# Kernel tuning notes

Hardware: AMD Instinct MI355X
Metric: run time of the kernel (lower is better)

Reference implementation:

```python
import jax, jax.numpy as jnp
import numpy as np

NB, NLOC, NALL = 1, 1024, 1024
NNEI, A_SEL = 64, 16
N_DIM, E_DIM, A_DIM, AXIS = 128, 64, 32, 4
UPD = 0.1  # update_residual, init 'const'


def _mlp_params(key, din, dout):
    kw, kb = jax.random.split(key)
    s = np.float32(1.0 / np.sqrt(din + dout))
    return (jax.random.normal(kw, (din, dout), jnp.float32) * s,
            jax.random.normal(kb, (dout,), jnp.float32) * s)


def setup_inputs() -> dict:
    key = jax.random.key(0)
    ks = jax.random.split(key, 16)
    inp = {}
    inp['node_ebd_ext'] = jax.random.normal(ks[0], (NB, NALL, N_DIM), jnp.float32)
    inp['edge_ebd'] = jax.random.normal(ks[1], (NB, NLOC, NNEI, E_DIM), jnp.float32)
    inp['h2'] = jax.random.normal(ks[2], (NB, NLOC, NNEI, 3), jnp.float32)
    inp['angle_ebd'] = jax.random.normal(ks[3], (NB, NLOC, A_SEL, A_SEL, A_DIM), jnp.float32)
    inp['nlist'] = jax.random.randint(ks[4], (NB, NLOC, NNEI), 0, NALL)
    inp['nlist_mask'] = jnp.ones((NB, NLOC, NNEI), bool)
    inp['sw'] = jax.random.uniform(ks[5], (NB, NLOC, NNEI), jnp.float32)
    inp['a_nlist_mask'] = jnp.ones((NB, NLOC, A_SEL), bool)
    inp['a_sw'] = jax.random.uniform(ks[6], (NB, NLOC, A_SEL), jnp.float32)
    n_sym_dim = AXIS * (N_DIM + E_DIM)          # 768
    edge_info_dim = 2 * N_DIM + E_DIM           # 320
    angle_dim = A_DIM + N_DIM + 2 * E_DIM       # 288 (a_compress_rate == 0)
    inp['w_node_self'], inp['b_node_self'] = _mlp_params(ks[7], N_DIM, N_DIM)
    inp['w_node_sym'], inp['b_node_sym'] = _mlp_params(ks[8], n_sym_dim, N_DIM)
    inp['w_node_edge'], inp['b_node_edge'] = _mlp_params(ks[9], edge_info_dim, N_DIM)
    inp['w_edge_self'], inp['b_edge_self'] = _mlp_params(ks[10], edge_info_dim, E_DIM)
    inp['w_ea1'], inp['b_ea1'] = _mlp_params(ks[11], angle_dim, E_DIM)
    inp['w_ea2'], inp['b_ea2'] = _mlp_params(ks[12], E_DIM, E_DIM)
    inp['w_angle_self'], inp['b_angle_self'] = _mlp_params(ks[13], angle_dim, A_DIM)
    inp['res_n0'] = UPD * jnp.ones((N_DIM,), jnp.float32)
    inp['res_n1'] = UPD * jnp.ones((N_DIM,), jnp.float32)
    inp['res_n2'] = UPD * jnp.ones((N_DIM,), jnp.float32)
    inp['res_e0'] = UPD * jnp.ones((E_DIM,), jnp.float32)
    inp['res_e1'] = UPD * jnp.ones((E_DIM,), jnp.float32)
    inp['res_a0'] = UPD * jnp.ones((A_DIM,), jnp.float32)
    return inp


def reference(node_ebd_ext, edge_ebd, h2, angle_ebd, nlist, nlist_mask, sw,
              a_nlist_mask, a_sw,
              w_node_self, b_node_self, w_node_sym, b_node_sym,
              w_node_edge, b_node_edge, w_edge_self, b_edge_self,
              w_ea1, b_ea1, w_ea2, b_ea2, w_angle_self, b_angle_self,
              res_n0, res_n1, res_n2, res_e0, res_e1, res_a0):
    act = jax.nn.silu
    nb, nloc, nnei, e_dim = edge_ebd.shape
    n_dim = node_ebd_ext.shape[-1]
    node_ebd = node_ebd_ext[:, :nloc]                      # nb x nloc x n_dim
    msw = nlist_mask.astype(edge_ebd.dtype) * sw           # nb x nloc x nnei

    # --- node self update ---
    node_self = act(node_ebd @ w_node_self + b_node_self)

    # --- gather neighbor node embeddings (nb x nloc x nnei x n_dim) ---
    idx = nlist.reshape(nb, nloc * nnei)
    nei_node = jnp.take_along_axis(node_ebd_ext, idx[:, :, None], axis=1)
    nei_node = nei_node.reshape(nb, nloc, nnei, n_dim)

    # --- symmetrization (GRRG invariants) ---
    inv_sqrt_nnei = 1.0 / np.sqrt(np.float32(nnei))
    def sym(ebd):
        g = ebd * msw[..., None]
        h2g2 = jnp.einsum('blnc,blnd->blcd', h2, g) * inv_sqrt_nnei  # nb,nloc,3,d
        grrg = jnp.einsum('blca,blcd->blad', h2g2[..., :AXIS], h2g2) / 3.0
        return grrg.reshape(nb, nloc, AXIS * ebd.shape[-1])
    node_sym = act(jnp.concatenate([sym(edge_ebd), sym(nei_node)], -1)
                   @ w_node_sym + b_node_sym)

    # --- edge info: [node_i, node_j, edge] (nb x nloc x nnei x 320) ---
    node_i = jnp.broadcast_to(node_ebd[:, :, None], (nb, nloc, nnei, n_dim))
    edge_info = jnp.concatenate([node_i, nei_node, edge_ebd], -1)

    # --- node <- edge message ---
    node_edge = (act(edge_info @ w_node_edge + b_node_edge) * sw[..., None]).sum(2) / nnei

    n_updated = node_ebd + res_n0 * node_self + res_n1 * node_sym + res_n2 * node_edge

    # --- edge self update ---
    edge_self = act(edge_info @ w_edge_self + b_edge_self)

    # --- angle info (nb x nloc x a_sel x a_sel x 288) ---
    ea = edge_ebd[:, :, :A_SEL] * a_nlist_mask.astype(edge_ebd.dtype)[..., None]
    node_a = jnp.broadcast_to(node_ebd[:, :, None, None], (nb, nloc, A_SEL, A_SEL, n_dim))
    ea_i = jnp.broadcast_to(ea[:, :, None], (nb, nloc, A_SEL, A_SEL, e_dim))
    ea_j = jnp.broadcast_to(ea[:, :, :, None], (nb, nloc, A_SEL, A_SEL, e_dim))
    angle_info = jnp.concatenate([angle_ebd, node_a, ea_i, ea_j], -1)

    # --- edge <- angle message ---
    eau = act(angle_info @ w_ea1 + b_ea1)
    weighted = a_sw[:, :, :, None, None] * a_sw[:, :, None, :, None] * eau
    reduced = weighted.sum(3) / np.sqrt(np.float32(A_SEL))   # nb,nloc,a_sel,e_dim
    padded = jnp.concatenate(
        [reduced, jnp.zeros((nb, nloc, nnei - A_SEL, e_dim), edge_ebd.dtype)], 2)
    full_mask = jnp.concatenate(
        [a_nlist_mask, jnp.zeros((nb, nloc, nnei - A_SEL), bool)], -1)
    padded = jnp.where(full_mask[..., None], padded, edge_ebd)  # smooth_edge_update=False
    e_angle = act(padded @ w_ea2 + b_ea2)

    e_updated = edge_ebd + res_e0 * edge_self + res_e1 * e_angle

    # --- angle self update ---
    angle_self = act(angle_info @ w_angle_self + b_angle_self)
    a_updated = angle_ebd + res_a0 * angle_self

    return n_updated, e_updated, a_updated
```

## Files before the change

kernel.cpp:

```cpp
#include <hip/hip_runtime.h>
#include <math.h>


typedef __attribute__((ext_vector_type(8))) __bf16 bf16x8;
typedef __attribute__((ext_vector_type(4))) float f32x4;
typedef __attribute__((ext_vector_type(8))) unsigned short us8;

__device__ __forceinline__ float silu(float x) { return x / (1.0f + __expf(-x)); }
__device__ __forceinline__ unsigned short f2bf(float x) {
    union { float f; unsigned int u; } v; v.f = x;
    unsigned int r = v.u + 0x7fffu + ((v.u >> 16) & 1u);
    return (unsigned short)(r >> 16);
}
__device__ __forceinline__ float bf2f(unsigned short h) {
    union { unsigned int u; float f; } v; v.u = ((unsigned int)h) << 16;
    return v.f;
}
__device__ __forceinline__ f32x4 MFMA(bf16x8 a, bf16x8 b, f32x4 c) {
    return __builtin_amdgcn_mfma_f32_16x16x32_bf16(a, b, c, 0, 0, 0);
}

#define OFF_NE  0
#define OFF_ES  24576
#define OFF_E2  36864
#define OFF_A1  40960
#define OFF_AS  43008
#define OFF_EJ1 44032
#define OFF_EI1 48128
#define OFF_EJ2 52224
#define OFF_EI2 54272
#define WS_UNITS 7040

#define P2_NSB  0
#define P2_NEB  16384
#define P2_ESB  32768
#define P2_NSYM 40960
#define P2_UNITS 17408
#define SCR2_BYTES  278528
#define BASES_BYTES 1310720
#define SYMB_BYTES  1572864
#define WS_NEEDED   3274752

__global__ __launch_bounds__(256) void prepAll(
    const float* __restrict__ w_ne, const float* __restrict__ w_es,
    const float* __restrict__ w_e2, const float* __restrict__ w_a1,
    const float* __restrict__ w_as, const float* __restrict__ w_ns,
    const float* __restrict__ w_nsym,
    unsigned short* __restrict__ wsb, unsigned short* __restrict__ scr2)
{
    if (blockIdx.x < 28) {
        int u = blockIdx.x * 256 + threadIdx.x;
        if (u >= WS_UNITS) return;
        const float* w; int N, k0, KS; int uu = u;
        if (uu < 3072)      { w = w_ne; N = 128; k0 = 128; KS = 6; }
        else if (uu < 4608) { uu -= 3072; w = w_es; N = 64;  k0 = 128; KS = 6; }
        else if (uu < 5120) { uu -= 4608; w = w_e2; N = 64;  k0 = 0;   KS = 2; }
        else if (uu < 5376) { uu -= 5120; w = w_a1; N = 64;  k0 = 0;   KS = 1; }
        else if (uu < 5504) { uu -= 5376; w = w_as; N = 32;  k0 = 0;   KS = 1; }
        else if (uu < 6016) { uu -= 5504; w = w_a1; N = 64;  k0 = 160; KS = 2; }
        else if (uu < 6528) { uu -= 6016; w = w_a1; N = 64;  k0 = 224; KS = 2; }
        else if (uu < 6784) { uu -= 6528; w = w_as; N = 32;  k0 = 160; KS = 2; }
        else                { uu -= 6784; w = w_as; N = 32;  k0 = 224; KS = 2; }
        int lane = uu & 63, rest = uu >> 6;
        int ks = rest % KS, nt = rest / KS;
        int k = k0 + ks * 32 + ((lane >> 4) << 3);
        int n = nt * 16 + (lane & 15);
        us8 o;
        #pragma unroll
        for (int t = 0; t < 8; ++t) o[t] = f2bf(w[(size_t)(k + t) * N + n]);
        *(us8*)&wsb[(size_t)u * 8] = o;
    } else {
        int u = (blockIdx.x - 28) * 256 + threadIdx.x;
        if (u >= P2_UNITS) return;
        const float* w; int N, KS; int uu = u;
        if (uu < 2048)      { w = w_ns;   N = 128; KS = 4; }
        else if (uu < 4096) { uu -= 2048; w = w_ne;   N = 128; KS = 4; }
        else if (uu < 5120) { uu -= 4096; w = w_es;   N = 64;  KS = 4; }
        else                { uu -= 5120; w = w_nsym; N = 128; KS = 24; }
        int lane = uu & 63, rest = uu >> 6;
        int ks = rest % KS, nt = rest / KS;
        int k = ks * 32 + ((lane >> 4) << 3);
        int n = nt * 16 + (lane & 15);
        us8 o;
        #pragma unroll
        for (int t = 0; t < 8; ++t) o[t] = f2bf(w[(size_t)(k + t) * N + n]);
        *(us8*)&scr2[(size_t)u * 8] = o;
    }
}

__global__ __launch_bounds__(256) void kernelBases(
    const float* __restrict__ node_ext, const unsigned short* __restrict__ scr2,
    const float* __restrict__ b_ns, const float* __restrict__ b_ne,
    const float* __restrict__ b_es, float* __restrict__ bases)
{
    __shared__ __align__(16) unsigned short s_N[16][136];
    const int b = blockIdx.x, tid = threadIdx.x, L0 = b * 16;
    for (int v = tid; v < 2048; v += 256)
        s_N[v >> 7][v & 127] = f2bf(node_ext[(size_t)(L0 + (v >> 7)) * 128 + (v & 127)]);
    __syncthreads();
    const int wv = tid >> 6, ln = tid & 63, lg = ln >> 4, lr = ln & 15;
    f32x4 acc[5];
    #pragma unroll
    for (int n = 0; n < 5; ++n) acc[n] = (f32x4){0.f,0.f,0.f,0.f};
    #pragma unroll
    for (int ks = 0; ks < 4; ++ks) {
        bf16x8 a = *(const bf16x8*)&s_N[lr][ks*32 + lg*8];
        #pragma unroll
        for (int ntl = 0; ntl < 5; ++ntl) {
            int t = wv * 5 + ntl;
            size_t eoff;
            if      (t < 8)  eoff = P2_NSB + (size_t)((t*4+ks)*64+ln)*8;
            else if (t < 16) eoff = P2_NEB + (size_t)(((t-8)*4+ks)*64+ln)*8;
            else             eoff = P2_ESB + (size_t)(((t-16)*4+ks)*64+ln)*8;
            bf16x8 bb = *(const bf16x8*)&scr2[eoff];
            acc[ntl] = MFMA(a, bb, acc[ntl]);
        }
    }
    #pragma unroll
    for (int ntl = 0; ntl < 5; ++ntl) {
        int t = wv * 5 + ntl;
        int col = t * 16 + lr;
        float bias = (col < 128) ? b_ns[col] : (col < 256) ? b_ne[col-128] : b_es[col-256];
        #pragma unroll
        for (int r = 0; r < 4; ++r)
            bases[(size_t)(L0 + lg*4 + r) * 320 + col] = acc[ntl][r] + bias;
    }
}

__global__ __launch_bounds__(512, 8) void kernelA(
    const float* __restrict__ node_ext, const float* __restrict__ edge,
    const float* __restrict__ h2, const int* __restrict__ nlist,
    const float* __restrict__ sw, const unsigned short* __restrict__ wsb,
    const float* __restrict__ bases, unsigned short* __restrict__ symb,
    const float* __restrict__ b_ea2,
    const float* __restrict__ res_n0, const float* __restrict__ res_n2,
    const float* __restrict__ res_e0, const float* __restrict__ res_e1,
    float* __restrict__ out_n, float* __restrict__ out_e)
{
    __shared__ __align__(16) unsigned short s_X[64][200];
    __shared__ float s_h2g2[3][192];
    __shared__ float s_base[320];
    __shared__ float s_ne[128];
    __shared__ float s_nodef[128];
    __shared__ float s_sw[64];
    __shared__ float s_h2w[192];
    __shared__ int   s_nl[64];

    const int l = blockIdx.x, tid = threadIdx.x;

    if (tid < 64) {
        s_nl[tid] = nlist[l*64 + tid];
        s_base[256 + tid] = bases[(size_t)l * 320 + 256 + tid];
    }
    else if (tid < 192) s_nodef[tid - 64] = node_ext[(size_t)l*128 + (tid - 64)];
    else if (tid < 256) s_sw[tid - 192] = sw[l*64 + (tid - 192)];
    else s_base[tid - 256] = bases[(size_t)l * 320 + (tid - 256)];
    __syncthreads();

    for (int v = tid; v < 8192; v += 512) {
        int n = v >> 7, j = v & 127;
        s_X[n][j] = f2bf(node_ext[(size_t)s_nl[n] * 128 + j]);
    }
    for (int v = tid; v < 4096; v += 512)
        s_X[v >> 6][128 + (v & 63)] = f2bf(edge[(size_t)l * 4096 + v]);
    if (tid < 192) s_h2w[tid] = h2[(size_t)l * 192 + tid] * s_sw[tid / 3];
    __syncthreads();

    for (int v = tid; v < 576; v += 512) {
        int c = v / 192, d = v % 192;
        float p0 = 0.f, p1 = 0.f, p2 = 0.f, p3 = 0.f;
        for (int n = 0; n < 64; n += 4) {
            p0 = fmaf(s_h2w[n * 3 + c],       bf2f(s_X[n][d]),     p0);
            p1 = fmaf(s_h2w[(n + 1) * 3 + c], bf2f(s_X[n + 1][d]), p1);
            p2 = fmaf(s_h2w[(n + 2) * 3 + c], bf2f(s_X[n + 2][d]), p2);
            p3 = fmaf(s_h2w[(n + 3) * 3 + c], bf2f(s_X[n + 3][d]), p3);
        }
        s_h2g2[c][d] = ((p0 + p1) + (p2 + p3)) * 0.125f;
    }
    __syncthreads();

    const int wv = tid >> 6, ln = tid & 63, lg = ln >> 4, lr = ln & 15;

    {
        f32x4 acc[4];
        #pragma unroll
        for (int m = 0; m < 4; ++m) acc[m] = (f32x4){0.f, 0.f, 0.f, 0.f};
        #pragma unroll
        for (int ks = 0; ks < 6; ++ks) {
            bf16x8 b = *(const bf16x8*)&wsb[OFF_NE + (size_t)((wv * 6 + ks) * 64 + ln) * 8];
            #pragma unroll
            for (int m = 0; m < 4; ++m) {
                bf16x8 a = *(const bf16x8*)&s_X[m * 16 + lr][ks * 32 + lg * 8];
                acc[m] = MFMA(a, b, acc[m]);
            }
        }
        int col = wv * 16 + lr;
        float base = s_base[128 + col];
        float cs = 0.f;
        #pragma unroll
        for (int m = 0; m < 4; ++m)
            #pragma unroll
            for (int r = 0; r < 4; ++r)
                cs = fmaf(silu(base + acc[m][r]), s_sw[m * 16 + lg * 4 + r], cs);
        cs += __shfl_xor(cs, 16);
        cs += __shfl_xor(cs, 32);
        if (lg == 0) s_ne[col] = cs;
    }

    {
        const int nt = wv >> 1, m0 = (wv & 1) * 2;
        f32x4 aes[2], ae2[2];
        #pragma unroll
        for (int mm = 0; mm < 2; ++mm) {
            aes[mm] = (f32x4){0.f, 0.f, 0.f, 0.f};
            ae2[mm] = (f32x4){0.f, 0.f, 0.f, 0.f};
        }
        #pragma unroll
        for (int ks = 0; ks < 6; ++ks) {
            bf16x8 b = *(const bf16x8*)&wsb[OFF_ES + (size_t)((nt * 6 + ks) * 64 + ln) * 8];
            bf16x8 a[2];
            #pragma unroll
            for (int mm = 0; mm < 2; ++mm)
                a[mm] = *(const bf16x8*)&s_X[(m0 + mm) * 16 + lr][ks * 32 + lg * 8];
            #pragma unroll
            for (int mm = 0; mm < 2; ++mm) aes[mm] = MFMA(a[mm], b, aes[mm]);
            if (ks >= 4) {
                bf16x8 b2 = *(const bf16x8*)&wsb[OFF_E2 + (size_t)((nt * 2 + (ks - 4)) * 64 + ln) * 8];
                #pragma unroll
                for (int mm = 0; mm < 2; ++mm)
                    if (m0 + mm > 0) ae2[mm] = MFMA(a[mm], b2, ae2[mm]);
            }
        }
        int o = nt * 16 + lr;
        float esb = s_base[256 + o];
        float re0 = res_e0[o], re1 = res_e1[o], be2 = b_ea2[o];
        #pragma unroll
        for (int mm = 0; mm < 2; ++mm) {
            int m = m0 + mm;
            #pragma unroll
            for (int r = 0; r < 4; ++r) {
                int n = m * 16 + lg * 4 + r;
                size_t gi = (size_t)l * 4096 + (size_t)n * 64 + o;
                float val = bf2f(s_X[n][128 + o]) + re0 * silu(esb + aes[mm][r]);
                if (m > 0) val = fmaf(re1, silu(be2 + ae2[mm][r]), val);
                out_e[gi] = val;
            }
        }
    }

    for (int v = tid; v < 768; v += 512) {
        float p;
        if (v < 256) {
            int a = v >> 6, d = v & 63;
            p = s_h2g2[0][128 + a] * s_h2g2[0][128 + d]
              + s_h2g2[1][128 + a] * s_h2g2[1][128 + d]
              + s_h2g2[2][128 + a] * s_h2g2[2][128 + d];
        } else {
            int v2 = v - 256; int a = v2 >> 7, d = v2 & 127;
            p = s_h2g2[0][a] * s_h2g2[0][d]
              + s_h2g2[1][a] * s_h2g2[1][d]
              + s_h2g2[2][a] * s_h2g2[2][d];
        }
        symb[(size_t)l * 768 + v] = f2bf(p * (1.f / 3.f));
    }
    __syncthreads();

    if (tid < 128) {
        float ne = s_ne[tid] * (1.f / 64.f);
        float v = s_nodef[tid];
        v = fmaf(res_n0[tid], silu(s_base[tid]), v);
        v = fmaf(res_n2[tid], ne, v);
        out_n[(size_t)l * 128 + tid] = v;
    }
}

__global__ __launch_bounds__(256) void kernelNsym(
    const unsigned short* __restrict__ symb, const unsigned short* __restrict__ scr2,
    const float* __restrict__ b_nsym, const float* __restrict__ res_n1,
    float* __restrict__ out_n)
{
    const int b = blockIdx.x, tid = threadIdx.x, L0 = b * 16;
    const int wv = tid >> 6, ln = tid & 63, lg = ln >> 4, lr = ln & 15;
    f32x4 acc[2];
    acc[0] = (f32x4){0.f,0.f,0.f,0.f};
    acc[1] = (f32x4){0.f,0.f,0.f,0.f};
    for (int ks = 0; ks < 24; ++ks) {
        bf16x8 a = *(const bf16x8*)&symb[(size_t)(L0 + lr) * 768 + ks*32 + lg*8];
        #pragma unroll
        for (int nt = 0; nt < 2; ++nt) {
            bf16x8 bb = *(const bf16x8*)&scr2[P2_NSYM + (size_t)(((wv*2+nt)*24+ks)*64+ln)*8];
            acc[nt] = MFMA(a, bb, acc[nt]);
        }
    }
    #pragma unroll
    for (int nt = 0; nt < 2; ++nt) {
        int col = (wv*2 + nt) * 16 + lr;
        float bias = b_nsym[col], rn = res_n1[col];
        #pragma unroll
        for (int r = 0; r < 4; ++r) {
            size_t idx = (size_t)(L0 + lg*4 + r) * 128 + col;
            out_n[idx] += rn * silu(acc[nt][r] + bias);
        }
    }
}

__global__ __launch_bounds__(512, 8) void kernelB(
    const float* __restrict__ node_ext, const float* __restrict__ edge,
    const float* __restrict__ angle, const float* __restrict__ a_sw,
    const unsigned short* __restrict__ wsb,
    const float* __restrict__ w_ea1, const float* __restrict__ b_ea1,
    const float* __restrict__ b_ea2,
    const float* __restrict__ w_angle_self, const float* __restrict__ b_angle_self,
    const float* __restrict__ res_e1, const float* __restrict__ res_a0,
    float* __restrict__ out_e, float* __restrict__ out_a)
{
    __shared__ __align__(16) unsigned short s_ea[16][72];
    __shared__ __align__(16) unsigned short s_redb[16][72];
    __shared__ float s_ej1[16][66];
    __shared__ float s_ei1[16][64];
    __shared__ float s_ej2[16][34];
    __shared__ float s_ei2[16][32];
    __shared__ float s_nt1[64];
    __shared__ float s_nt2[32];
    __shared__ float s_asw[16];
    __shared__ float s_nodef[128];

    const int l = blockIdx.x, tid = threadIdx.x;
    const int wv = tid >> 6, ln = tid & 63, lg = ln >> 4, lr = ln & 15;

    bf16x8 a[2];
    #pragma unroll
    for (int mm = 0; mm < 2; ++mm) {
        const float* ap = angle + (size_t)l * 8192
                        + (size_t)((wv * 2 + mm) * 16 + lr) * 32 + lg * 8;
        float4 f0 = *(const float4*)ap;
        float4 f1 = *(const float4*)(ap + 4);
        bf16x8 t;
        t[0] = (__bf16)f0.x; t[1] = (__bf16)f0.y; t[2] = (__bf16)f0.z; t[3] = (__bf16)f0.w;
        t[4] = (__bf16)f1.x; t[5] = (__bf16)f1.y; t[6] = (__bf16)f1.z; t[7] = (__bf16)f1.w;
        a[mm] = t;
    }

    if (tid < 128) s_nodef[tid] = node_ext[(size_t)l * 128 + tid];
    else if (tid < 144) s_asw[tid - 128] = a_sw[l * 16 + (tid - 128)];
    for (int v = tid; v < 1024; v += 512) s_ea[v >> 6][v & 63] = f2bf(edge[(size_t)l * 4096 + v]);
    __syncthreads();

    if (wv < 6) {
        bf16x8 a0 = *(const bf16x8*)&s_ea[lr][lg * 8];
        bf16x8 a1 = *(const bf16x8*)&s_ea[lr][32 + lg * 8];
        if (wv < 2) {
            #pragma unroll
            for (int ntl = 0; ntl < 2; ++ntl) {
                int nt = wv * 2 + ntl;
                f32x4 c = (f32x4){0.f, 0.f, 0.f, 0.f};
                c = MFMA(a0, *(const bf16x8*)&wsb[OFF_EJ1 + (size_t)((nt * 2 + 0) * 64 + ln) * 8], c);
                c = MFMA(a1, *(const bf16x8*)&wsb[OFF_EJ1 + (size_t)((nt * 2 + 1) * 64 + ln) * 8], c);
                #pragma unroll
                for (int r = 0; r < 4; ++r) s_ej1[lg * 4 + r][nt * 16 + lr] = c[r];
            }
        } else if (wv < 4) {
            #pragma unroll
            for (int ntl = 0; ntl < 2; ++ntl) {
                int nt = (wv - 2) * 2 + ntl;
                f32x4 c = (f32x4){0.f, 0.f, 0.f, 0.f};
                c = MFMA(a0, *(const bf16x8*)&wsb[OFF_EI1 + (size_t)((nt * 2 + 0) * 64 + ln) * 8], c);
                c = MFMA(a1, *(const bf16x8*)&wsb[OFF_EI1 + (size_t)((nt * 2 + 1) * 64 + ln) * 8], c);
                #pragma unroll
                for (int r = 0; r < 4; ++r) s_ei1[lg * 4 + r][nt * 16 + lr] = c[r];
            }
        } else if (wv == 4) {
            #pragma unroll
            for (int nt = 0; nt < 2; ++nt) {
                f32x4 c = (f32x4){0.f, 0.f, 0.f, 0.f};
                c = MFMA(a0, *(const bf16x8*)&wsb[OFF_EJ2 + (size_t)((nt * 2 + 0) * 64 + ln) * 8], c);
                c = MFMA(a1, *(const bf16x8*)&wsb[OFF_EJ2 + (size_t)((nt * 2 + 1) * 64 + ln) * 8], c);
                #pragma unroll
                for (int r = 0; r < 4; ++r) s_ej2[lg * 4 + r][nt * 16 + lr] = c[r];
            }
        } else {
            #pragma unroll
            for (int nt = 0; nt < 2; ++nt) {
                f32x4 c = (f32x4){0.f, 0.f, 0.f, 0.f};
                c = MFMA(a0, *(const bf16x8*)&wsb[OFF_EI2 + (size_t)((nt * 2 + 0) * 64 + ln) * 8], c);
                c = MFMA(a1, *(const bf16x8*)&wsb[OFF_EI2 + (size_t)((nt * 2 + 1) * 64 + ln) * 8], c);
                #pragma unroll
                for (int r = 0; r < 4; ++r) s_ei2[lg * 4 + r][nt * 16 + lr] = c[r];
            }
        }
    } else if (wv == 6) {
        float p = b_ea1[ln];
        for (int k = 0; k < 128; ++k) p = fmaf(s_nodef[k], w_ea1[(32 + k) * 64 + ln], p);
        s_nt1[ln] = p;
    } else {
        if (ln < 32) {
            float p = b_angle_self[ln];
            for (int k = 0; k < 128; ++k) p = fmaf(s_nodef[k], w_angle_self[(32 + k) * 32 + ln], p);
            s_nt2[ln] = p;
        }
    }
    __syncthreads();

    #pragma unroll
    for (int nt = 0; nt < 4; ++nt) {
        bf16x8 b = *(const bf16x8*)&wsb[OFF_A1 + (size_t)(nt * 64 + ln) * 8];
        #pragma unroll
        for (int mm = 0; mm < 2; ++mm) {
            f32x4 c = MFMA(a[mm], b, (f32x4){0.f, 0.f, 0.f, 0.f});
            int i = wv * 2 + mm;
            int o = nt * 16 + lr;
            float b0 = s_nt1[o] + s_ei1[i][o];
            float ps = 0.f;
            #pragma unroll
            for (int r = 0; r < 4; ++r) {
                int jj = lg * 4 + r;
                ps = fmaf(silu(c[r] + b0 + s_ej1[jj][o]), s_asw[jj], ps);
            }
            ps += __shfl_xor(ps, 16);
            ps += __shfl_xor(ps, 32);
            if (lg == 0) s_redb[i][o] = f2bf(ps * s_asw[i] * 0.25f);
        }
    }
    #pragma unroll
    for (int nt = 0; nt < 2; ++nt) {
        bf16x8 b = *(const bf16x8*)&wsb[OFF_AS + (size_t)(nt * 64 + ln) * 8];
        #pragma unroll
        for (int mm = 0; mm < 2; ++mm) {
            f32x4 c = MFMA(a[mm], b, (f32x4){0.f, 0.f, 0.f, 0.f});
            int i = wv * 2 + mm;
            int o = nt * 16 + lr;
            float b0 = s_nt2[o] + s_ei2[i][o];
            float ra = res_a0[o];
            #pragma unroll
            for (int r = 0; r < 4; ++r) {
                int jj = lg * 4 + r;
                size_t gi = (size_t)l * 8192 + (size_t)(i * 16 + jj) * 32 + o;
                out_a[gi] = angle[gi] + ra * silu(c[r] + b0 + s_ej2[jj][o]);
            }
        }
    }
    __syncthreads();

    if (wv < 4) {
        bf16x8 a0 = *(const bf16x8*)&s_redb[lr][lg * 8];
        bf16x8 a1 = *(const bf16x8*)&s_redb[lr][32 + lg * 8];
        const int nt = wv;
        f32x4 c = (f32x4){0.f, 0.f, 0.f, 0.f};
        c = MFMA(a0, *(const bf16x8*)&wsb[OFF_E2 + (size_t)((nt * 2 + 0) * 64 + ln) * 8], c);
        c = MFMA(a1, *(const bf16x8*)&wsb[OFF_E2 + (size_t)((nt * 2 + 1) * 64 + ln) * 8], c);
        int o = nt * 16 + lr;
        float be = b_ea2[o], re1 = res_e1[o];
        #pragma unroll
        for (int r = 0; r < 4; ++r) {
            int n = lg * 4 + r;
            size_t gi = (size_t)l * 4096 + (size_t)n * 64 + o;
            out_e[gi] += re1 * silu(be + c[r]);
        }
    }
}

extern "C" void kernel_launch(void* const* d_in, const int* in_sizes, int n_in,
                              void* d_out, int out_size, void* d_ws, size_t ws_size,
                              hipStream_t stream)
{
    const float* node_ext     = (const float*)d_in[0];
    const float* edge         = (const float*)d_in[1];
    const float* h2           = (const float*)d_in[2];
    const float* angle        = (const float*)d_in[3];
    const int*   nlist        = (const int*)d_in[4];
    const float* sw           = (const float*)d_in[6];
    const float* a_sw         = (const float*)d_in[8];
    const float* w_node_self  = (const float*)d_in[9];
    const float* b_node_self  = (const float*)d_in[10];
    const float* w_node_sym   = (const float*)d_in[11];
    const float* b_node_sym   = (const float*)d_in[12];
    const float* w_node_edge  = (const float*)d_in[13];
    const float* b_node_edge  = (const float*)d_in[14];
    const float* w_edge_self  = (const float*)d_in[15];
    const float* b_edge_self  = (const float*)d_in[16];
    const float* w_ea1        = (const float*)d_in[17];
    const float* b_ea1        = (const float*)d_in[18];
    const float* w_ea2        = (const float*)d_in[19];
    const float* b_ea2        = (const float*)d_in[20];
    const float* w_angle_self = (const float*)d_in[21];
    const float* b_angle_self = (const float*)d_in[22];
    const float* res_n0       = (const float*)d_in[23];
    const float* res_n1       = (const float*)d_in[24];
    const float* res_n2       = (const float*)d_in[25];
    const float* res_e0       = (const float*)d_in[26];
    const float* res_e1       = (const float*)d_in[27];
    const float* res_a0       = (const float*)d_in[28];

    float* out_n = (float*)d_out;
    float* out_e = out_n + 1024 * 128;
    float* out_a = out_e + 1024 * 64 * 64;
    unsigned short* wsb = (unsigned short*)d_ws;

    char* scrbase = (ws_size >= (size_t)WS_NEEDED) ? ((char*)d_ws + 112640)
                                                   : (char*)out_a;
    unsigned short* scr2 = (unsigned short*)scrbase;
    float* bases = (float*)(scrbase + SCR2_BYTES);
    unsigned short* symb = (unsigned short*)(scrbase + SCR2_BYTES + BASES_BYTES);
    (void)in_sizes; (void)n_in; (void)out_size;

    hipLaunchKernelGGL(prepAll, dim3(96), dim3(256), 0, stream,
        w_node_edge, w_edge_self, w_ea2, w_ea1, w_angle_self, w_node_self, w_node_sym,
        wsb, scr2);

    hipLaunchKernelGGL(kernelBases, dim3(64), dim3(256), 0, stream,
        node_ext, scr2, b_node_self, b_node_edge, b_edge_self, bases);

    hipLaunchKernelGGL(kernelA, dim3(1024), dim3(512), 0, stream,
        node_ext, edge, h2, nlist, sw, wsb, bases, symb, b_ea2,
        res_n0, res_n2, res_e0, res_e1, out_n, out_e);

    hipLaunchKernelGGL(kernelNsym, dim3(64), dim3(256), 0, stream,
        symb, scr2, b_node_sym, res_n1, out_n);

    hipLaunchKernelGGL(kernelB, dim3(1024), dim3(512), 0, stream,
        node_ext, edge, angle, a_sw, wsb,
        w_ea1, b_ea1, b_ea2, w_angle_self, b_angle_self,
        res_e1, res_a0, out_e, out_a);
}
```

Baseline: 78.66 us.

## Fold node-sym GEMM into kernelB and precompute per-node angle terms in bases

The per-node angle projection terms (node_ebd @ w_ea1 and node_ebd @ w_angle_self slices) move into the batched MFMA bases kernel, so kernelB no longer runs scalar 128-long dot products in two waves. The separate kernelNsym launch is folded into kernelB as 64 extra blocks, removing one launch, and kernelA gathers with float4 loads. This costs a larger workspace and a fallback path when the workspace is too small, and the extra blocks share kernelB's 512-thread shape and LDS footprint.

After: 81.06 us. 1.03x slower.

```diff
diff --git a/kernel.cpp b/kernel.cpp
--- a/kernel.cpp
+++ b/kernel.cpp
@@ -35,11 +35,13 @@
 #define P2_NEB  16384
 #define P2_ESB  32768
 #define P2_NSYM 40960
-#define P2_UNITS 17408
-#define SCR2_BYTES  278528
-#define BASES_BYTES 1310720
+#define P2_NT1  139264
+#define P2_NT2  147456
+#define P2_UNITS 18944
+#define SCR2_BYTES  303104
+#define BASES_BYTES 1703936
 #define SYMB_BYTES  1572864
-#define WS_NEEDED   3274752
+#define WS_NEEDED   3692544
 
 __global__ __launch_bounds__(256) void prepAll(
     const float* __restrict__ w_ne, const float* __restrict__ w_es,
@@ -72,14 +74,16 @@
     } else {
         int u = (blockIdx.x - 28) * 256 + threadIdx.x;
         if (u >= P2_UNITS) return;
-        const float* w; int N, KS; int uu = u;
-        if (uu < 2048)      { w = w_ns;   N = 128; KS = 4; }
-        else if (uu < 4096) { uu -= 2048; w = w_ne;   N = 128; KS = 4; }
-        else if (uu < 5120) { uu -= 4096; w = w_es;   N = 64;  KS = 4; }
-        else                { uu -= 5120; w = w_nsym; N = 128; KS = 24; }
+        const float* w; int N, k0, KS; int uu = u;
+        if (uu < 2048)       { w = w_ns;   N = 128; k0 = 0;  KS = 4; }
+        else if (uu < 4096)  { uu -= 2048;  w = w_ne;   N = 128; k0 = 0;  KS = 4; }
+        else if (uu < 5120)  { uu -= 4096;  w = w_es;   N = 64;  k0 = 0;  KS = 4; }
+        else if (uu < 17408) { uu -= 5120;  w = w_nsym; N = 128; k0 = 0;  KS = 24; }
+        else if (uu < 18432) { uu -= 17408; w = w_a1;   N = 64;  k0 = 32; KS = 4; }
+        else                 { uu -= 18432; w = w_as;   N = 32;  k0 = 32; KS = 4; }
         int lane = uu & 63, rest = uu >> 6;
         int ks = rest % KS, nt = rest / KS;
-        int k = ks * 32 + ((lane >> 4) << 3);
+        int k = k0 + ks * 32 + ((lane >> 4) << 3);
         int n = nt * 16 + (lane & 15);
         us8 o;
         #pragma unroll
@@ -91,7 +95,8 @@
 __global__ __launch_bounds__(256) void kernelBases(
     const float* __restrict__ node_ext, const unsigned short* __restrict__ scr2,
     const float* __restrict__ b_ns, const float* __restrict__ b_ne,
-    const float* __restrict__ b_es, float* __restrict__ bases)
+    const float* __restrict__ b_es, const float* __restrict__ b_ea1,
+    const float* __restrict__ b_as, float* __restrict__ bases)
 {
     __shared__ __align__(16) unsigned short s_N[16][136];
     const int b = blockIdx.x, tid = threadIdx.x, L0 = b * 16;
@@ -99,31 +104,37 @@
         s_N[v >> 7][v & 127] = f2bf(node_ext[(size_t)(L0 + (v >> 7)) * 128 + (v & 127)]);
     __syncthreads();
     const int wv = tid >> 6, ln = tid & 63, lg = ln >> 4, lr = ln & 15;
-    f32x4 acc[5];
-    #pragma unroll
-    for (int n = 0; n < 5; ++n) acc[n] = (f32x4){0.f,0.f,0.f,0.f};
+    f32x4 acc[7];
+    #pragma unroll
+    for (int n = 0; n < 7; ++n) acc[n] = (f32x4){0.f,0.f,0.f,0.f};
     #pragma unroll
     for (int ks = 0; ks < 4; ++ks) {
         bf16x8 a = *(const bf16x8*)&s_N[lr][ks*32 + lg*8];
         #pragma unroll
-        for (int ntl = 0; ntl < 5; ++ntl) {
-            int t = wv * 5 + ntl;
+        for (int ntl = 0; ntl < 7; ++ntl) {
+            int t = wv * 7 + ntl;
+            if (t >= 26) continue;
             size_t eoff;
             if      (t < 8)  eoff = P2_NSB + (size_t)((t*4+ks)*64+ln)*8;
             else if (t < 16) eoff = P2_NEB + (size_t)(((t-8)*4+ks)*64+ln)*8;
-            else             eoff = P2_ESB + (size_t)(((t-16)*4+ks)*64+ln)*8;
+            else if (t < 20) eoff = P2_ESB + (size_t)(((t-16)*4+ks)*64+ln)*8;
+            else if (t < 24) eoff = P2_NT1 + (size_t)(((t-20)*4+ks)*64+ln)*8;
+            else             eoff = P2_NT2 + (size_t)(((t-24)*4+ks)*64+ln)*8;
             bf16x8 bb = *(const bf16x8*)&scr2[eoff];
             acc[ntl] = MFMA(a, bb, acc[ntl]);
         }
     }
     #pragma unroll
-    for (int ntl = 0; ntl < 5; ++ntl) {
-        int t = wv * 5 + ntl;
+    for (int ntl = 0; ntl < 7; ++ntl) {
+        int t = wv * 7 + ntl;
+        if (t >= 26) continue;
         int col = t * 16 + lr;
-        float bias = (col < 128) ? b_ns[col] : (col < 256) ? b_ne[col-128] : b_es[col-256];
+        float bias = (col < 128) ? b_ns[col] : (col < 256) ? b_ne[col-128]
+                   : (col < 320) ? b_es[col-256] : (col < 384) ? b_ea1[col-320]
+                   : b_as[col-384];
         #pragma unroll
         for (int r = 0; r < 4; ++r)
-            bases[(size_t)(L0 + lg*4 + r) * 320 + col] = acc[ntl][r] + bias;
+            bases[(size_t)(L0 + lg*4 + r) * 416 + col] = acc[ntl][r] + bias;
     }
 }
 
@@ -150,19 +161,25 @@
 
     if (tid < 64) {
         s_nl[tid] = nlist[l*64 + tid];
-        s_base[256 + tid] = bases[(size_t)l * 320 + 256 + tid];
+        s_base[256 + tid] = bases[(size_t)l * 416 + 256 + tid];
     }
     else if (tid < 192) s_nodef[tid - 64] = node_ext[(size_t)l*128 + (tid - 64)];
     else if (tid < 256) s_sw[tid - 192] = sw[l*64 + (tid - 192)];
-    else s_base[tid - 256] = bases[(size_t)l * 320 + (tid - 256)];
-    __syncthreads();
-
-    for (int v = tid; v < 8192; v += 512) {
-        int n = v >> 7, j = v & 127;
-        s_X[n][j] = f2bf(node_ext[(size_t)s_nl[n] * 128 + j]);
-    }
-    for (int v = tid; v < 4096; v += 512)
-        s_X[v >> 6][128 + (v & 63)] = f2bf(edge[(size_t)l * 4096 + v]);
+    else s_base[tid - 256] = bases[(size_t)l * 416 + (tid - 256)];
+    __syncthreads();
+
+    for (int v = tid; v < 2048; v += 512) {
+        int n = v >> 5, c4 = (v & 31) * 4;
+        float4 f = *(const float4*)&node_ext[(size_t)s_nl[n] * 128 + c4];
+        s_X[n][c4+0] = f2bf(f.x); s_X[n][c4+1] = f2bf(f.y);
+        s_X[n][c4+2] = f2bf(f.z); s_X[n][c4+3] = f2bf(f.w);
+    }
+    for (int v = tid; v < 1024; v += 512) {
+        int n = v >> 4, c4 = (v & 15) * 4;
+        float4 f = *(const float4*)&edge[(size_t)l * 4096 + n * 64 + c4];
+        s_X[n][128+c4+0] = f2bf(f.x); s_X[n][128+c4+1] = f2bf(f.y);
+        s_X[n][128+c4+2] = f2bf(f.z); s_X[n][128+c4+3] = f2bf(f.w);
+    }
     if (tid < 192) s_h2w[tid] = h2[(size_t)l * 192 + tid] * s_sw[tid / 3];
     __syncthreads();
 
@@ -307,13 +324,36 @@
 __global__ __launch_bounds__(512, 8) void kernelB(
     const float* __restrict__ node_ext, const float* __restrict__ edge,
     const float* __restrict__ angle, const float* __restrict__ a_sw,
-    const unsigned short* __restrict__ wsb,
+    const unsigned short* __restrict__ wsb, const float* __restrict__ bases,
+    const unsigned short* __restrict__ symb, const unsigned short* __restrict__ scr2,
     const float* __restrict__ w_ea1, const float* __restrict__ b_ea1,
-    const float* __restrict__ b_ea2,
     const float* __restrict__ w_angle_self, const float* __restrict__ b_angle_self,
-    const float* __restrict__ res_e1, const float* __restrict__ res_a0,
-    float* __restrict__ out_e, float* __restrict__ out_a)
+    const float* __restrict__ b_nsym, const float* __restrict__ res_n1,
+    const float* __restrict__ b_ea2, const float* __restrict__ res_e1,
+    const float* __restrict__ res_a0, const int use_bases_nt,
+    float* __restrict__ out_n, float* __restrict__ out_e, float* __restrict__ out_a)
 {
+    const int bid = blockIdx.x, tid = threadIdx.x;
+    const int wv = tid >> 6, ln = tid & 63, lg = ln >> 4, lr = ln & 15;
+
+    if (bid >= 1024) {
+        const int L0 = (bid - 1024) * 16;
+        f32x4 acc = (f32x4){0.f,0.f,0.f,0.f};
+        for (int ks = 0; ks < 24; ++ks) {
+            bf16x8 a = *(const bf16x8*)&symb[(size_t)(L0 + lr) * 768 + ks*32 + lg*8];
+            bf16x8 bb = *(const bf16x8*)&scr2[P2_NSYM + (size_t)((wv*24+ks)*64+ln)*8];
+            acc = MFMA(a, bb, acc);
+        }
+        int col = wv * 16 + lr;
+        float bias = b_nsym[col], rn = res_n1[col];
+        #pragma unroll
+        for (int r = 0; r < 4; ++r) {
+            size_t idx = (size_t)(L0 + lg*4 + r) * 128 + col;
+            out_n[idx] += rn * silu(acc[r] + bias);
+        }
+        return;
+    }
+
     __shared__ __align__(16) unsigned short s_ea[16][72];
     __shared__ __align__(16) unsigned short s_redb[16][72];
     __shared__ float s_ej1[16][66];
@@ -325,8 +365,7 @@
     __shared__ float s_asw[16];
     __shared__ float s_nodef[128];
 
-    const int l = blockIdx.x, tid = threadIdx.x;
-    const int wv = tid >> 6, ln = tid & 63, lg = ln >> 4, lr = ln & 15;
+    const int l = bid;
 
     bf16x8 a[2];
     #pragma unroll
@@ -343,47 +382,39 @@
 
     if (tid < 128) s_nodef[tid] = node_ext[(size_t)l * 128 + tid];
     else if (tid < 144) s_asw[tid - 128] = a_sw[l * 16 + (tid - 128)];
+    else if (use_bases_nt) {
+        if (tid >= 192 && tid < 256) s_nt1[tid - 192] = bases[(size_t)l * 416 + 320 + (tid - 192)];
+        else if (tid >= 256 && tid < 288) s_nt2[tid - 256] = bases[(size_t)l * 416 + 384 + (tid - 256)];
+    }
     for (int v = tid; v < 1024; v += 512) s_ea[v >> 6][v & 63] = f2bf(edge[(size_t)l * 4096 + v]);
     __syncthreads();
 
-    if (wv < 6) {
+    if (use_bases_nt || wv < 6) {
         bf16x8 a0 = *(const bf16x8*)&s_ea[lr][lg * 8];
         bf16x8 a1 = *(const bf16x8*)&s_ea[lr][32 + lg * 8];
-        if (wv < 2) {
-            #pragma unroll
-            for (int ntl = 0; ntl < 2; ++ntl) {
-                int nt = wv * 2 + ntl;
-                f32x4 c = (f32x4){0.f, 0.f, 0.f, 0.f};
-                c = MFMA(a0, *(const bf16x8*)&wsb[OFF_EJ1 + (size_t)((nt * 2 + 0) * 64 + ln) * 8], c);
-                c = MFMA(a1, *(const bf16x8*)&wsb[OFF_EJ1 + (size_t)((nt * 2 + 1) * 64 + ln) * 8], c);
+        const int stride = use_bases_nt ? 8 : 6;
+        for (int pass = 0; pass < 2; ++pass) {
+            int j = wv + pass * stride;
+            if (j >= 12) break;
+            f32x4 c = (f32x4){0.f, 0.f, 0.f, 0.f};
+            size_t base;
+            int nt;
+            if      (j < 4)  { base = OFF_EJ1; nt = j; }
+            else if (j < 8)  { base = OFF_EI1; nt = j - 4; }
+            else if (j < 10) { base = OFF_EJ2; nt = j - 8; }
+            else             { base = OFF_EI2; nt = j - 10; }
+            c = MFMA(a0, *(const bf16x8*)&wsb[base + (size_t)((nt * 2 + 0) * 64 + ln) * 8], c);
+            c = MFMA(a1, *(const bf16x8*)&wsb[base + (size_t)((nt * 2 + 1) * 64 + ln) * 8], c);
+            if (j < 4) {
                 #pragma unroll
                 for (int r = 0; r < 4; ++r) s_ej1[lg * 4 + r][nt * 16 + lr] = c[r];
-            }
-        } else if (wv < 4) {
-            #pragma unroll
-            for (int ntl = 0; ntl < 2; ++ntl) {
-                int nt = (wv - 2) * 2 + ntl;
-                f32x4 c = (f32x4){0.f, 0.f, 0.f, 0.f};
-                c = MFMA(a0, *(const bf16x8*)&wsb[OFF_EI1 + (size_t)((nt * 2 + 0) * 64 + ln) * 8], c);
-                c = MFMA(a1, *(const bf16x8*)&wsb[OFF_EI1 + (size_t)((nt * 2 + 1) * 64 + ln) * 8], c);
+            } else if (j < 8) {
                 #pragma unroll
                 for (int r = 0; r < 4; ++r) s_ei1[lg * 4 + r][nt * 16 + lr] = c[r];
-            }
-        } else if (wv == 4) {
-            #pragma unroll
-            for (int nt = 0; nt < 2; ++nt) {
-                f32x4 c = (f32x4){0.f, 0.f, 0.f, 0.f};
-                c = MFMA(a0, *(const bf16x8*)&wsb[OFF_EJ2 + (size_t)((nt * 2 + 0) * 64 + ln) * 8], c);
-                c = MFMA(a1, *(const bf16x8*)&wsb[OFF_EJ2 + (size_t)((nt * 2 + 1) * 64 + ln) * 8], c);
+            } else if (j < 10) {
                 #pragma unroll
                 for (int r = 0; r < 4; ++r) s_ej2[lg * 4 + r][nt * 16 + lr] = c[r];
-            }
-        } else {
-            #pragma unroll
-            for (int nt = 0; nt < 2; ++nt) {
-                f32x4 c = (f32x4){0.f, 0.f, 0.f, 0.f};
-                c = MFMA(a0, *(const bf16x8*)&wsb[OFF_EI2 + (size_t)((nt * 2 + 0) * 64 + ln) * 8], c);
-                c = MFMA(a1, *(const bf16x8*)&wsb[OFF_EI2 + (size_t)((nt * 2 + 1) * 64 + ln) * 8], c);
+            } else {
                 #pragma unroll
                 for (int r = 0; r < 4; ++r) s_ei2[lg * 4 + r][nt * 16 + lr] = c[r];
             }
@@ -496,29 +527,36 @@
     float* out_a = out_e + 1024 * 64 * 64;
     unsigned short* wsb = (unsigned short*)d_ws;
 
-    char* scrbase = (ws_size >= (size_t)WS_NEEDED) ? ((char*)d_ws + 112640)
-                                                   : (char*)out_a;
+    const bool ws_fits = (ws_size >= (size_t)WS_NEEDED);
+    char* scrbase = ws_fits ? ((char*)d_ws + 112640) : (char*)out_a;
     unsigned short* scr2 = (unsigned short*)scrbase;
     float* bases = (float*)(scrbase + SCR2_BYTES);
     unsigned short* symb = (unsigned short*)(scrbase + SCR2_BYTES + BASES_BYTES);
     (void)in_sizes; (void)n_in; (void)out_size;
 
-    hipLaunchKernelGGL(prepAll, dim3(96), dim3(256), 0, stream,
+    hipLaunchKernelGGL(prepAll, dim3(102), dim3(256), 0, stream,
         w_node_edge, w_edge_self, w_ea2, w_ea1, w_angle_self, w_node_self, w_node_sym,
         wsb, scr2);
 
     hipLaunchKernelGGL(kernelBases, dim3(64), dim3(256), 0, stream,
-        node_ext, scr2, b_node_self, b_node_edge, b_edge_self, bases);
+        node_ext, scr2, b_node_self, b_node_edge, b_edge_self, b_ea1, b_angle_self,
+        bases);
 
     hipLaunchKernelGGL(kernelA, dim3(1024), dim3(512), 0, stream,
         node_ext, edge, h2, nlist, sw, wsb, bases, symb, b_ea2,
         res_n0, res_n2, res_e0, res_e1, out_n, out_e);
 
-    hipLaunchKernelGGL(kernelNsym, dim3(64), dim3(256), 0, stream,
-        symb, scr2, b_node_sym, res_n1, out_n);
-
-    hipLaunchKernelGGL(kernelB, dim3(1024), dim3(512), 0, stream,
-        node_ext, edge, angle, a_sw, wsb,
-        w_ea1, b_ea1, b_ea2, w_angle_self, b_angle_self,
-        res_e1, res_a0, out_e, out_a);
-}
+    if (ws_fits) {
+        hipLaunchKernelGGL(kernelB, dim3(1088), dim3(512), 0, stream,
+            node_ext, edge, angle, a_sw, wsb, bases, symb, scr2,
+            w_ea1, b_ea1, w_angle_self, b_angle_self, b_node_sym, res_n1,
+            b_ea2, res_e1, res_a0, 1, out_n, out_e, out_a);
+    } else {
+        hipLaunchKernelGGL(kernelNsym, dim3(64), dim3(256), 0, stream,
+            symb, scr2, b_node_sym, res_n1, out_n);
+        hipLaunchKernelGGL(kernelB, dim3(1024), dim3(512), 0, stream,
+            node_ext, edge, angle, a_sw, wsb, bases, symb, scr2,
+            w_ea1, b_ea1, w_angle_self, b_angle_self, b_node_sym, res_n1,
+            b_ea2, res_e1, res_a0, 0, out_n, out_e, out_a);
+    }
+}
```
